# Kernel tuning notes

Measured on AMD Instinct MI355X. Metric: run time of the kernel, lower is better.

## Reference

```python
import jax, jax.numpy as jnp
import numpy as np

SEQ, D = 4096, 1024  # vector_size == dimension == 1024


def setup_inputs() -> dict:
    key = jax.random.key(0)
    ks = jax.random.split(key, 7)
    s = 1.0 / np.sqrt(D)
    return {
        "X": jax.random.normal(ks[0], (SEQ, D), dtype=jnp.float32),
        "Wq": jax.random.normal(ks[1], (D, D), dtype=jnp.float32) * s,
        "bq": jax.random.normal(ks[2], (D,), dtype=jnp.float32) * s,
        "Wk": jax.random.normal(ks[3], (D, D), dtype=jnp.float32) * s,
        "bk": jax.random.normal(ks[4], (D,), dtype=jnp.float32) * s,
        "Wv": jax.random.normal(ks[5], (D, D), dtype=jnp.float32) * s,
        "bv": jax.random.normal(ks[6], (D,), dtype=jnp.float32) * s,
    }


def reference(X, Wq, bq, Wk, bk, Wv, bv):
    # Batched QKV projections (nn.Linear: x @ W^T + b), replacing the per-vector loop.
    Q = X @ Wq.T + bq            # [S, D]
    K = X @ Wk.T + bk            # [S, D]
    V = X @ Wv.T + bv            # [S, D]
    scale = 1.0 / jnp.sqrt(jnp.asarray(D, dtype=X.dtype))
    scores = (Q @ K.T) * scale   # [S, S]
    attn = jax.nn.softmax(scores, axis=1)
    return attn @ V              # [S, D]
```

## Files before the change

### kernel.cpp

```cpp
#include <hip/hip_runtime.h>
#include <hip/hip_bf16.h>
#include <stdint.h>


typedef __bf16 bf16_t;
typedef __bf16 bf16x4 __attribute__((ext_vector_type(4)));
typedef __bf16 bf16x8 __attribute__((ext_vector_type(8)));
typedef float f32x4 __attribute__((ext_vector_type(4)));

#define AS1 __attribute__((address_space(1)))
#define AS3 __attribute__((address_space(3)))

__device__ __forceinline__ void async_ld16(const void* g, void* l) {
  __builtin_amdgcn_global_load_lds((AS1 void*)g, (AS3 void*)l, 16, 0, 0);
}

template <int MODE, int BN>
__global__ __launch_bounds__(256, 2) void gemm_k(
    const bf16_t* __restrict__ A, const bf16_t* __restrict__ B, const int K,
    bf16_t* __restrict__ o0, bf16_t* __restrict__ o1, bf16_t* __restrict__ o2,
    const float* __restrict__ b0, const float* __restrict__ b1,
    const float* __restrict__ b2, float* __restrict__ fout,
    float* __restrict__ rowsum) {
  constexpr int NF = BN / 32;
  __shared__ bf16_t As[128 * 32];
  __shared__ bf16_t Bs[BN * 32];

  const int t = threadIdx.x;
  const int lane = t & 63;
  const int wave = t >> 6;
  const int wm = wave >> 1;
  const int wn = wave & 1;
  const int q = lane >> 4;
  const int l16 = lane & 15;
  const int wnoff = wn * (BN / 2);
  const int n0 = blockIdx.x * BN;
  const int m0 = blockIdx.y * 128;

  const f32x4 zero4 = {0.f, 0.f, 0.f, 0.f};
  f32x4 acc[4][NF];
#pragma unroll
  for (int i = 0; i < 4; ++i)
#pragma unroll
    for (int j = 0; j < NF; ++j) acc[i][j] = zero4;

  const int srow = t >> 2;
  const int schunk = (t & 3) ^ ((t >> 3) & 3);
  const bf16_t* Ab = A + (size_t)(m0 + srow) * K + schunk * 8;
  const bf16_t* Bb = B + (size_t)(n0 + srow) * K + schunk * 8;
  bf16_t* Asl = As + t * 8;
  bf16_t* Bsl = Bs + t * 8;

  const int xa = q ^ ((l16 >> 1) & 3);
  const int ar = wm * 64 + l16;
  const int br = wnoff + l16;

  for (int kt = 0; kt < K; kt += 32) {
    async_ld16(Ab + kt, Asl);
    async_ld16(Ab + (size_t)64 * K + kt, Asl + 2048);
    async_ld16(Bb + kt, Bsl);
    if constexpr (BN == 128) async_ld16(Bb + (size_t)64 * K + kt, Bsl + 2048);
    __syncthreads();

    bf16x8 fa[4], fb[NF];
#pragma unroll
    for (int im = 0; im < 4; ++im)
      fa[im] = *(const bf16x8*)(As + (ar + im * 16) * 32 + xa * 8);
#pragma unroll
    for (int j = 0; j < NF; ++j)
      fb[j] = *(const bf16x8*)(Bs + (br + j * 16) * 32 + xa * 8);
#pragma unroll
    for (int im = 0; im < 4; ++im)
#pragma unroll
      for (int j = 0; j < NF; ++j)
        acc[im][j] = __builtin_amdgcn_mfma_f32_16x16x32_bf16(
            fa[im], fb[j], acc[im][j], 0, 0, 0);
    __syncthreads();
  }

  const int mBase = m0 + wm * 64 + q * 4;

  if constexpr (MODE == 0) {
    const int sel = n0 >> 10;
    const int nl0 = (n0 & 1023) + wnoff + l16;
    const float* bias = (sel == 0) ? b0 : ((sel == 1) ? b1 : b2);
    const float sc = (sel == 0) ? 0.03125f : 1.0f;
#pragma unroll
    for (int j = 0; j < NF; ++j) {
      const int nl = nl0 + j * 16;
      const float bb = bias[nl];
#pragma unroll
      for (int im = 0; im < 4; ++im) {
        const int mr = mBase + im * 16;
        if (sel < 2) {
          bf16_t* dst = (sel == 0) ? o0 : o1;
#pragma unroll
          for (int r = 0; r < 4; ++r)
            dst[(size_t)(mr + r) * 1024 + nl] =
                (bf16_t)((acc[im][j][r] + bb) * sc);
        } else {
          bf16x4 v;
#pragma unroll
          for (int r = 0; r < 4; ++r) v[r] = (bf16_t)(acc[im][j][r] + bb);
          *(bf16x4*)(o2 + (size_t)nl * 4096 + mr) = v;
        }
      }
    }
  } else if constexpr (MODE == 1) {
    float ps[4][4];
#pragma unroll
    for (int im = 0; im < 4; ++im)
#pragma unroll
      for (int r = 0; r < 4; ++r) ps[im][r] = 0.f;
#pragma unroll
    for (int j = 0; j < NF; ++j) {
      const int n = n0 + wnoff + j * 16 + l16;
#pragma unroll
      for (int im = 0; im < 4; ++im) {
        const int mr = mBase + im * 16;
#pragma unroll
        for (int r = 0; r < 4; ++r) {
          const float e = __expf(acc[im][j][r]);
          ps[im][r] += e;
          o0[(size_t)(mr + r) * 4096 + n] = (bf16_t)e;
        }
      }
    }
#pragma unroll
    for (int im = 0; im < 4; ++im)
#pragma unroll
      for (int r = 0; r < 4; ++r) {
        float v = ps[im][r];
        v += __shfl_xor(v, 1);
        v += __shfl_xor(v, 2);
        v += __shfl_xor(v, 4);
        v += __shfl_xor(v, 8);
        ps[im][r] = v;
      }
    if (l16 == 0) {
#pragma unroll
      for (int im = 0; im < 4; ++im)
#pragma unroll
        for (int r = 0; r < 4; ++r)
          atomicAdd(rowsum + mBase + im * 16 + r, ps[im][r]);
    }
  } else {
#pragma unroll
    for (int im = 0; im < 4; ++im) {
      const int mr = mBase + im * 16;
      float inv[4];
#pragma unroll
      for (int r = 0; r < 4; ++r) inv[r] = 1.0f / rowsum[mr + r];
#pragma unroll
      for (int j = 0; j < NF; ++j) {
        const int n = n0 + wnoff + j * 16 + l16;
#pragma unroll
        for (int r = 0; r < 4; ++r)
          fout[(size_t)(mr + r) * 1024 + n] = acc[im][j][r] * inv[r];
      }
    }
  }
}

__global__ __launch_bounds__(256) void cvt_all(
    const float* __restrict__ X, const float* __restrict__ Wq,
    const float* __restrict__ Wk, const float* __restrict__ Wv,
    bf16_t* __restrict__ Xb, bf16_t* __restrict__ Wb) {
  int i = blockIdx.x * 256 + threadIdx.x;
  const float* src;
  bf16_t* dst;
  int off;
  if (i < 1048576) {
    src = X; dst = Xb; off = i;
  } else {
    const int w = i - 1048576;
    const int sel = w >> 18;
    off = w & 0x3FFFF;
    src = (sel == 0) ? Wq : ((sel == 1) ? Wk : Wv);
    dst = Wb + (size_t)sel * (1024 * 1024);
  }
  const float4 v = ((const float4*)src)[off];
  bf16x4 o;
  o[0] = (bf16_t)v.x; o[1] = (bf16_t)v.y; o[2] = (bf16_t)v.z; o[3] = (bf16_t)v.w;
  ((bf16x4*)dst)[off] = o;
}

__global__ __launch_bounds__(256) void zero_f32(float* __restrict__ p, int n) {
  const int i = blockIdx.x * 256 + threadIdx.x;
  if (i < n) p[i] = 0.f;
}

extern "C" void kernel_launch(void* const* d_in, const int* in_sizes, int n_in,
                              void* d_out, int out_size, void* d_ws,
                              size_t ws_size, hipStream_t stream) {
  const int S = 4096, D = 1024;
  const float* X  = (const float*)d_in[0];
  const float* Wq = (const float*)d_in[1];
  const float* bq = (const float*)d_in[2];
  const float* Wk = (const float*)d_in[3];
  const float* bk = (const float*)d_in[4];
  const float* Wv = (const float*)d_in[5];
  const float* bv = (const float*)d_in[6];
  float* out = (float*)d_out;

  bf16_t* Xb = (bf16_t*)d_ws;
  bf16_t* Wb = Xb + (size_t)S * D;
  bf16_t* Qb = Wb + (size_t)3 * D * D;
  bf16_t* Kb = Qb + (size_t)S * D;
  bf16_t* Vt = Kb + (size_t)S * D;
  bf16_t* Sc = Vt + (size_t)D * S;
  float* rowsum = (float*)(Sc + (size_t)S * S);

  cvt_all<<<7168, 256, 0, stream>>>(X, Wq, Wk, Wv, Xb, Wb);
  zero_f32<<<16, 256, 0, stream>>>(rowsum, S);

  gemm_k<0, 128><<<dim3(3 * D / 128, S / 128), 256, 0, stream>>>(
      Xb, Wb, D, Qb, Kb, Vt, bq, bk, bv, nullptr, nullptr);
  gemm_k<1, 128><<<dim3(S / 128, S / 128), 256, 0, stream>>>(
      Qb, Kb, D, Sc, nullptr, nullptr, nullptr, nullptr, nullptr, nullptr,
      rowsum);
  gemm_k<2, 64><<<dim3(D / 64, S / 128), 256, 0, stream>>>(
      Sc, Vt, S, nullptr, nullptr, nullptr, nullptr, nullptr, nullptr, out,
      rowsum);
}
```

Before: 244.3 us.

## Split-K the attention-times-V GEMM with atomic accumulation and wider tiles

The final P@V GEMM is split over the 4096-long reduction into four chunks via a third grid dimension. Each block accumulates its partial product into the output with float atomics, and the output is zeroed by a new kernel beforehand. Tile width also grows from 64 to 128 columns for better operand reuse. This adds atomic traffic and an extra zeroing pass in exchange for more parallelism and shorter serial K loops.

After: 264.7 us. 8.4% more time.

```diff
diff --git a/kernel.cpp b/kernel.cpp
--- a/kernel.cpp
+++ b/kernel.cpp
@@ -17,7 +17,8 @@
 
 template <int MODE, int BN>
 __global__ __launch_bounds__(256, 2) void gemm_k(
-    const bf16_t* __restrict__ A, const bf16_t* __restrict__ B, const int K,
+    const bf16_t* __restrict__ A, const bf16_t* __restrict__ B, const int ld,
+    const int Klen,
     bf16_t* __restrict__ o0, bf16_t* __restrict__ o1, bf16_t* __restrict__ o2,
     const float* __restrict__ b0, const float* __restrict__ b1,
     const float* __restrict__ b2, float* __restrict__ fout,
@@ -36,6 +37,7 @@
   const int wnoff = wn * (BN / 2);
   const int n0 = blockIdx.x * BN;
   const int m0 = blockIdx.y * 128;
+  const int k0 = blockIdx.z * Klen;
 
   const f32x4 zero4 = {0.f, 0.f, 0.f, 0.f};
   f32x4 acc[4][NF];
@@ -46,8 +48,8 @@
 
   const int srow = t >> 2;
   const int schunk = (t & 3) ^ ((t >> 3) & 3);
-  const bf16_t* Ab = A + (size_t)(m0 + srow) * K + schunk * 8;
-  const bf16_t* Bb = B + (size_t)(n0 + srow) * K + schunk * 8;
+  const bf16_t* Ab = A + (size_t)(m0 + srow) * ld + k0 + schunk * 8;
+  const bf16_t* Bb = B + (size_t)(n0 + srow) * ld + k0 + schunk * 8;
   bf16_t* Asl = As + t * 8;
   bf16_t* Bsl = Bs + t * 8;
 
@@ -55,11 +57,11 @@
   const int ar = wm * 64 + l16;
   const int br = wnoff + l16;
 
-  for (int kt = 0; kt < K; kt += 32) {
+  for (int kt = 0; kt < Klen; kt += 32) {
     async_ld16(Ab + kt, Asl);
-    async_ld16(Ab + (size_t)64 * K + kt, Asl + 2048);
+    async_ld16(Ab + (size_t)64 * ld + kt, Asl + 2048);
     async_ld16(Bb + kt, Bsl);
-    if constexpr (BN == 128) async_ld16(Bb + (size_t)64 * K + kt, Bsl + 2048);
+    if constexpr (BN == 128) async_ld16(Bb + (size_t)64 * ld + kt, Bsl + 2048);
     __syncthreads();
 
     bf16x8 fa[4], fb[NF];
@@ -156,7 +158,7 @@
         const int n = n0 + wnoff + j * 16 + l16;
 #pragma unroll
         for (int r = 0; r < 4; ++r)
-          fout[(size_t)(mr + r) * 1024 + n] = acc[im][j][r] * inv[r];
+          atomicAdd(fout + (size_t)(mr + r) * 1024 + n, acc[im][j][r] * inv[r]);
       }
     }
   }
@@ -190,6 +192,12 @@
   if (i < n) p[i] = 0.f;
 }
 
+__global__ __launch_bounds__(256) void zero_f32x4(float* __restrict__ p) {
+  const int i = blockIdx.x * 256 + threadIdx.x;
+  const float4 z = {0.f, 0.f, 0.f, 0.f};
+  ((float4*)p)[i] = z;
+}
+
 extern "C" void kernel_launch(void* const* d_in, const int* in_sizes, int n_in,
                               void* d_out, int out_size, void* d_ws,
                               size_t ws_size, hipStream_t stream) {
@@ -213,13 +221,14 @@
 
   cvt_all<<<7168, 256, 0, stream>>>(X, Wq, Wk, Wv, Xb, Wb);
   zero_f32<<<16, 256, 0, stream>>>(rowsum, S);
+  zero_f32x4<<<S * D / 4 / 256, 256, 0, stream>>>(out);
 
   gemm_k<0, 128><<<dim3(3 * D / 128, S / 128), 256, 0, stream>>>(
-      Xb, Wb, D, Qb, Kb, Vt, bq, bk, bv, nullptr, nullptr);
+      Xb, Wb, D, D, Qb, Kb, Vt, bq, bk, bv, nullptr, nullptr);
   gemm_k<1, 128><<<dim3(S / 128, S / 128), 256, 0, stream>>>(
-      Qb, Kb, D, Sc, nullptr, nullptr, nullptr, nullptr, nullptr, nullptr,
+      Qb, Kb, D, D, Sc, nullptr, nullptr, nullptr, nullptr, nullptr, nullptr,
       rowsum);
-  gemm_k<2, 64><<<dim3(D / 64, S / 128), 256, 0, stream>>>(
-      Sc, Vt, S, nullptr, nullptr, nullptr, nullptr, nullptr, nullptr, out,
+  gemm_k<2, 128><<<dim3(D / 128, S / 128, 4), 256, 0, stream>>>(
+      Sc, Vt, S, D, nullptr, nullptr, nullptr, nullptr, nullptr, nullptr, out,
       rowsum);
 }
```
